# Kernel tuning notes

Hardware: AMD Instinct MI355X
Metric: run time of the kernel (lower is better)

The kernel has to match this reference:

```python
import jax, jax.numpy as jnp
import numpy as np

NUM_HEADS = 16
HEAD_DIM = 64
D_MODEL = NUM_HEADS * HEAD_DIM
EPS = 1e-8
SCALE = 1.0 / np.sqrt(HEAD_DIM)


def setup_inputs() -> dict:
    key = jax.random.key(0)
    ks = jax.random.split(key, 5)
    B, S = 2, 2048
    w_std = 1.0 / np.sqrt(D_MODEL)
    return {
        "x": jax.random.normal(ks[0], (B, S, D_MODEL), dtype=jnp.float32),
        "Wq": jax.random.normal(ks[1], (D_MODEL, D_MODEL), dtype=jnp.float32) * w_std,
        "Wk": jax.random.normal(ks[2], (D_MODEL, D_MODEL), dtype=jnp.float32) * w_std,
        "Wv": jax.random.normal(ks[3], (D_MODEL, D_MODEL), dtype=jnp.float32) * w_std,
        "Wo": jax.random.normal(ks[4], (D_MODEL, D_MODEL), dtype=jnp.float32) * w_std,
        "xsa_scale": jnp.ones((1,), dtype=jnp.float32),
    }


def reference(x, Wq, Wk, Wv, Wo, xsa_scale):
    B, S, _ = x.shape
    # torch nn.Linear(no bias): y = x @ W.T
    def proj(W):
        y = jnp.einsum("bsd,ed->bse", x, W)
        # (B, S, D) -> (B, H, S, Dh)
        return y.reshape(B, S, NUM_HEADS, HEAD_DIM).transpose(0, 2, 1, 3)

    q, k, v = proj(Wq), proj(Wk), proj(Wv)
    scores = jnp.einsum("bhqd,bhkd->bhqk", q, k) * SCALE
    attn = jax.nn.softmax(scores, axis=-1)
    out = jnp.einsum("bhqk,bhkd->bhqd", attn, v)
    # subtract_projection: remove component of out along each token's own v
    dot = jnp.sum(out * v, axis=-1, keepdims=True)
    v_norm_sq = jnp.sum(v * v, axis=-1, keepdims=True) + EPS
    out = out - xsa_scale * (dot / v_norm_sq) * v
    out = out.transpose(0, 2, 1, 3).reshape(B, S, D_MODEL)
    return jnp.einsum("bsd,ed->bse", out, Wo)


if __name__ == "__main__":
    print(reference(**setup_inputs()).shape)
```

## Files before the change

### kernel.cpp

```cpp
#include <hip/hip_runtime.h>
#include <math.h>

#define BATCH 2
#define SEQ   2048
#define NH    16
#define HD    64
#define DM    1024
#define MROWS (BATCH * SEQ)
#define NEL   ((size_t)MROWS * DM)
#define WEL   ((size_t)DM * DM)
#define SM_SCALE_LOG2E 0.18033688011112042f

typedef __bf16 bf16x8 __attribute__((ext_vector_type(8)));
typedef float  f32x4  __attribute__((ext_vector_type(4)));

#define MFMA16(a, b, c) __builtin_amdgcn_mfma_f32_16x16x32_bf16((a), (b), (c), 0, 0, 0)
#define EXP2(x) __builtin_amdgcn_exp2f(x)

#define GLDS16(g, s) __builtin_amdgcn_global_load_lds( \
    (const __attribute__((address_space(1))) void*)(g), \
    (__attribute__((address_space(3))) void*)(s), 16, 0, 0)


__global__ __launch_bounds__(256) void cvt_x(const float* __restrict__ src,
                                             __bf16* __restrict__ dst) {
    const size_t i = ((size_t)blockIdx.x * 256 + threadIdx.x) * 4;
    const float4 f = *(const float4*)&src[i];
    __bf16 b[4] = {(__bf16)f.x, (__bf16)f.y, (__bf16)f.z, (__bf16)f.w};
    *(ushort4*)&dst[i] = *(ushort4*)b;
}

__global__ __launch_bounds__(256) void cvt_w(const float* __restrict__ w0,
                                             const float* __restrict__ w1,
                                             const float* __restrict__ w2,
                                             const float* __restrict__ w3,
                                             __bf16* __restrict__ dst) {
    const int z = blockIdx.z;
    const float* src = (z == 0) ? w0 : (z == 1) ? w1 : (z == 2) ? w2 : w3;
    __bf16* d = dst + (size_t)z * WEL;
    const size_t i = ((size_t)blockIdx.x * 256 + threadIdx.x) * 4;
    const float4 f = *(const float4*)&src[i];
    __bf16 b[4] = {(__bf16)f.x, (__bf16)f.y, (__bf16)f.z, (__bf16)f.w};
    *(ushort4*)&d[i] = *(ushort4*)b;
}

template<int BN>
__global__ __launch_bounds__(256) void gemm_nt_mfma(
    const __bf16* __restrict__ A, const __bf16* __restrict__ W0,
    void* __restrict__ C0, __bf16* __restrict__ Vt, int mode)
{
    constexpr int NI  = BN / 32;
    constexpr int NIT = DM / 32;
    __shared__ __bf16 Ast[2][128 * 32];
    __shared__ __bf16 Bst[2][BN * 32];

    const int t = threadIdx.x;
    const int w = t >> 6, l = t & 63;
    const int quad = l >> 4, l15 = l & 15;
    const int z = blockIdx.z;
    const int m0 = blockIdx.y * 128, n0 = blockIdx.x * BN;
    const int wm = (w >> 1) * 64, wn = (w & 1) * (BN / 2);

    const __bf16* Wp = W0 + (size_t)z * WEL;

    const int lrow = l >> 2;
    const int lkof = ((l & 3) ^ ((lrow >> 1) & 3)) * 8;
    const int qsw = (quad ^ ((l15 >> 1) & 3)) * 8;

    const __bf16* Ag = A + (size_t)(m0 + w * 32 + lrow) * DM + lkof;
    const int aoff = (w * 32) * 32;
    const int brow = (BN == 128) ? (w * 32) : (w * 16);
    const __bf16* Bg = Wp + (size_t)(n0 + brow + lrow) * DM + lkof;
    const int boff = brow * 32;

    f32x4 acc[4][NI];
    #pragma unroll
    for (int i = 0; i < 4; i++)
        #pragma unroll
        for (int j = 0; j < NI; j++) acc[i][j] = (f32x4)0.0f;

    GLDS16(Ag,           &Ast[0][aoff]);
    GLDS16(Ag + 16 * DM, &Ast[0][aoff + 512]);
    GLDS16(Bg,           &Bst[0][boff]);
    if (BN == 128) GLDS16(Bg + 16 * DM, &Bst[0][boff + 512]);
    __syncthreads();

    for (int i = 0; i < NIT; i++) {
        const int cur = i & 1, nxt = cur ^ 1;
        if (i + 1 < NIT) {
            const int k0 = (i + 1) * 32;
            GLDS16(Ag + k0,           &Ast[nxt][aoff]);
            GLDS16(Ag + k0 + 16 * DM, &Ast[nxt][aoff + 512]);
            GLDS16(Bg + k0,           &Bst[nxt][boff]);
            if (BN == 128) GLDS16(Bg + k0 + 16 * DM, &Bst[nxt][boff + 512]);
        }

        bf16x8 af[4], bfr[NI];
        #pragma unroll
        for (int mi = 0; mi < 4; mi++)
            af[mi] = *(const bf16x8*)&Ast[cur][(wm + mi * 16 + l15) * 32 + qsw];
        #pragma unroll
        for (int ni = 0; ni < NI; ni++)
            bfr[ni] = *(const bf16x8*)&Bst[cur][(wn + ni * 16 + l15) * 32 + qsw];
        #pragma unroll
        for (int mi = 0; mi < 4; mi++)
            #pragma unroll
            for (int ni = 0; ni < NI; ni++)
                acc[mi][ni] = MFMA16(af[mi], bfr[ni], acc[mi][ni]);

        __syncthreads();
    }

    if (mode) {
        const float sc = (z == 0) ? SM_SCALE_LOG2E : 1.0f;
        __bf16* C = (__bf16*)C0 + (size_t)z * NEL;
        #pragma unroll
        for (int mi = 0; mi < 4; mi++)
            #pragma unroll
            for (int ni = 0; ni < NI; ni++)
                #pragma unroll
                for (int r = 0; r < 4; r++) {
                    const int row = m0 + wm + mi * 16 + quad * 4 + r;
                    const int col = n0 + wn + ni * 16 + l15;
                    const int b = row >> 11, s = row & (SEQ - 1);
                    const int h = col >> 6,  d = col & (HD - 1);
                    const __bf16 val = (__bf16)(acc[mi][ni][r] * sc);
                    C[((size_t)(b * NH + h) * SEQ + s) * HD + d] = val;
                    if (z == 2)
                        Vt[((size_t)(b * NH + h) * HD + d) * SEQ + s] = val;
                }
    } else {
        float* C = (float*)C0;
        #pragma unroll
        for (int mi = 0; mi < 4; mi++)
            #pragma unroll
            for (int ni = 0; ni < NI; ni++)
                #pragma unroll
                for (int r = 0; r < 4; r++) {
                    const int row = m0 + wm + mi * 16 + quad * 4 + r;
                    const int col = n0 + wn + ni * 16 + l15;
                    C[(size_t)row * DM + col] = acc[mi][ni][r];
                }
    }
}

__global__ __launch_bounds__(256, 3) void attn_mfma(
    const __bf16* __restrict__ Q, const __bf16* __restrict__ K,
    const __bf16* __restrict__ Vt, const __bf16* __restrict__ V,
    const float* __restrict__ xsa, __bf16* __restrict__ X2)
{
    __shared__ __bf16 KV[2][2][2 * 64 * 32];
    __shared__ __bf16 Pt[4][32][64];

    const int t = threadIdx.x;
    const int w = t >> 6, l = t & 63;
    const int quad = l >> 4, l15 = l & 15;
    const int bh = blockIdx.x & 31;
    const int q0 = (blockIdx.x >> 5) * 128;

    const __bf16* Qb  = Q  + (size_t)bh * SEQ * HD;
    const __bf16* Kb  = K  + (size_t)bh * SEQ * HD;
    const __bf16* Vtb = Vt + (size_t)bh * HD * SEQ;

    const int lrow = l >> 2;
    const int lkof = ((l & 3) ^ ((lrow >> 1) & 3)) * 8;
    const int qsw = (quad ^ ((l15 >> 1) & 3)) * 8;
    const int pkey = l15 & 7;

    __bf16* Qst = &KV[1][0][0];
    #pragma unroll
    for (int h = 0; h < 2; h++)
        #pragma unroll
        for (int qq = 0; qq < 2; qq++)
            GLDS16(Qb + (size_t)(q0 + w * 32 + qq * 16 + lrow) * HD + h * 32 + lkof,
                   Qst + h * 4096 + (w * 32 + qq * 16) * 32);
    #pragma unroll
    for (int h = 0; h < 2; h++)
        GLDS16(Kb + (size_t)(w * 16 + lrow) * HD + h * 32 + lkof,
               &KV[0][0][h * 2048 + (w * 16) * 32]);
    #pragma unroll
    for (int kh = 0; kh < 2; kh++)
        GLDS16(Vtb + (size_t)(w * 16 + lrow) * SEQ + kh * 32 + lkof,
               &KV[0][1][kh * 2048 + (w * 16) * 32]);
    __syncthreads();

    bf16x8 qf[2][2];
    #pragma unroll
    for (int h = 0; h < 2; h++)
        #pragma unroll
        for (int mi = 0; mi < 2; mi++)
            qf[h][mi] = *(const bf16x8*)&Qst[h * 4096 +
                          (w * 32 + mi * 16 + l15) * 32 + qsw];
    __syncthreads();

    float l_i[2] = {0.0f, 0.0f};
    f32x4 o[2][4];
    #pragma unroll
    for (int mi = 0; mi < 2; mi++)
        #pragma unroll
        for (int db = 0; db < 4; db++) o[mi][db] = (f32x4)0.0f;

    constexpr int NT = SEQ / 64;
    for (int kt = 0; kt < NT; kt++) {
        const int cur = kt & 1, nxt = cur ^ 1;
        if (kt + 1 < NT) {
            const int k0n = (kt + 1) * 64;
            #pragma unroll
            for (int h = 0; h < 2; h++)
                GLDS16(Kb + (size_t)(k0n + w * 16 + lrow) * HD + h * 32 + lkof,
                       &KV[nxt][0][h * 2048 + (w * 16) * 32]);
            #pragma unroll
            for (int kh = 0; kh < 2; kh++)
                GLDS16(Vtb + (size_t)(w * 16 + lrow) * SEQ + k0n + kh * 32 + lkof,
                       &KV[nxt][1][kh * 2048 + (w * 16) * 32]);
        }
        const __bf16* Ks = &KV[cur][0][0];
        const __bf16* Vs = &KV[cur][1][0];

        f32x4 st[2][4];
        #pragma unroll
        for (int mi = 0; mi < 2; mi++)
            #pragma unroll
            for (int kb = 0; kb < 4; kb++) st[mi][kb] = (f32x4)0.0f;
        #pragma unroll
        for (int h = 0; h < 2; h++)
            #pragma unroll
            for (int kb = 0; kb < 4; kb++) {
                const bf16x8 kf = *(const bf16x8*)&Ks[h * 2048 +
                                      (kb * 16 + l15) * 32 + qsw];
                #pragma unroll
                for (int mi = 0; mi < 2; mi++)
                    st[mi][kb] = MFMA16(kf, qf[h][mi], st[mi][kb]);
            }

        #pragma unroll
        for (int mi = 0; mi < 2; mi++) {
            float rs = 0.0f;
            #pragma unroll
            for (int kb = 0; kb < 4; kb++)
                #pragma unroll
                for (int r = 0; r < 4; r++) {
                    const float p = EXP2(st[mi][kb][r]);
                    st[mi][kb][r] = p;
                    rs += p;
                }
            rs += __shfl_xor(rs, 16);
            rs += __shfl_xor(rs, 32);
            l_i[mi] += rs;
            #pragma unroll
            for (int kb = 0; kb < 4; kb++) {
                __bf16 pb[4] = {(__bf16)st[mi][kb][0], (__bf16)st[mi][kb][1],
                                (__bf16)st[mi][kb][2], (__bf16)st[mi][kb][3]};
                const int pc = ((kb * 2 + (quad >> 1)) ^ pkey) * 8 + (quad & 1) * 4;
                *(uint2*)&Pt[w][mi * 16 + l15][pc] = *(uint2*)pb;
            }
        }

        #pragma unroll
        for (int kh = 0; kh < 2; kh++) {
            bf16x8 pf[2];
            #pragma unroll
            for (int mi = 0; mi < 2; mi++) {
                const int pc = ((kh * 4 + quad) ^ pkey) * 8;
                pf[mi] = *(const bf16x8*)&Pt[w][mi * 16 + l15][pc];
            }
            #pragma unroll
            for (int db = 0; db < 4; db++) {
                const bf16x8 vf = *(const bf16x8*)&Vs[kh * 2048 +
                                      (db * 16 + l15) * 32 + qsw];
                #pragma unroll
                for (int mi = 0; mi < 2; mi++)
                    o[mi][db] = MFMA16(vf, pf[mi], o[mi][db]);
            }
        }

        __syncthreads();
    }

    const float xs = xsa[0];
    const int b = bh >> 4, h = bh & (NH - 1);
    const __bf16* Vb = V + (size_t)bh * SEQ * HD;
    #pragma unroll
    for (int mi = 0; mi < 2; mi++) {
        const int q = q0 + w * 32 + mi * 16 + l15;
        const float inv = 1.0f / l_i[mi];
        float vv[4][4], on[4][4];
        float dp = 0.0f, nn = 0.0f;
        #pragma unroll
        for (int db = 0; db < 4; db++) {
            __bf16 vb4[4];
            *(uint2*)vb4 = *(const uint2*)&Vb[(size_t)q * HD + db * 16 + quad * 4];
            #pragma unroll
            for (int r = 0; r < 4; r++) {
                const float vf = (float)vb4[r];
                const float of = o[mi][db][r] * inv;
                vv[db][r] = vf;
                on[db][r] = of;
                dp += of * vf;
                nn += vf * vf;
            }
        }
        dp += __shfl_xor(dp, 16); dp += __shfl_xor(dp, 32);
        nn += __shfl_xor(nn, 16); nn += __shfl_xor(nn, 32);
        const float coef = xs * dp / (nn + 1e-8f);
        #pragma unroll
        for (int db = 0; db < 4; db++) {
            __bf16 ob[4];
            #pragma unroll
            for (int r = 0; r < 4; r++)
                ob[r] = (__bf16)(on[db][r] - coef * vv[db][r]);
            *(uint2*)&X2[((size_t)b * SEQ + q) * DM + h * HD + db * 16 + quad * 4] =
                *(uint2*)ob;
        }
    }
}

extern "C" void kernel_launch(void* const* d_in, const int* in_sizes, int n_in,
                              void* d_out, int out_size, void* d_ws, size_t ws_size,
                              hipStream_t stream)
{
    (void)in_sizes; (void)n_in; (void)out_size; (void)ws_size;
    const float* x   = (const float*)d_in[0];
    const float* Wq  = (const float*)d_in[1];
    const float* Wk  = (const float*)d_in[2];
    const float* Wv  = (const float*)d_in[3];
    const float* Wo  = (const float*)d_in[4];
    const float* xsa = (const float*)d_in[5];
    float* out = (float*)d_out;

    __bf16* xb  = (__bf16*)d_ws;
    __bf16* Wb  = xb  + NEL;
    __bf16* Qb  = Wb  + 4 * WEL;
    __bf16* Kb  = Qb  + NEL;
    __bf16* Vb  = Kb  + NEL;
    __bf16* Vtb = Vb  + NEL;
    __bf16* X2  = Vtb + NEL;

    cvt_x<<<dim3(NEL / 1024), 256, 0, stream>>>(x, xb);
    cvt_w<<<dim3(WEL / 1024, 1, 4), 256, 0, stream>>>(Wq, Wk, Wv, Wo, Wb);

    gemm_nt_mfma<128><<<dim3(DM / 128, MROWS / 128, 3), 256, 0, stream>>>(
        xb, Wb, Qb, Vtb, 1);

    attn_mfma<<<dim3((SEQ / 128) * BATCH * NH), 256, 0, stream>>>(
        Qb, Kb, Vtb, Vb, xsa, X2);

    gemm_nt_mfma<64><<<dim3(DM / 64, MROWS / 128, 1), 256, 0, stream>>>(
        X2, Wb + 3 * WEL, out, nullptr, 0);
}
```

Measured before the change: 198.7 us.

## Fuse conversion kernels, add MFMA priority hints, halve attention block size

Merges the x and weight bf16 conversion kernels into a single launch to remove one kernel launch. Wraps the MFMA loops in the GEMM and attention kernels with s_setprio so matrix work gets issue priority over other waves. Shrinks attention blocks from 4 to 2 waves (64 queries per block), doubling the grid and having each wave load twice as many K/V rows per tile. The smaller blocks give more blocks for scheduling, but each K/V tile is reused by fewer queries, which raises global load traffic per query.

```diff
diff --git a/kernel.cpp b/kernel.cpp
--- a/kernel.cpp
+++ b/kernel.cpp
@@ -22,26 +22,29 @@
     (__attribute__((address_space(3))) void*)(s), 16, 0, 0)
 
 
-__global__ __launch_bounds__(256) void cvt_x(const float* __restrict__ src,
-                                             __bf16* __restrict__ dst) {
-    const size_t i = ((size_t)blockIdx.x * 256 + threadIdx.x) * 4;
+__global__ __launch_bounds__(256) void cvt_all(
+    const float* __restrict__ x,
+    const float* __restrict__ w0, const float* __restrict__ w1,
+    const float* __restrict__ w2, const float* __restrict__ w3,
+    __bf16* __restrict__ xb, __bf16* __restrict__ wb)
+{
+    const int bid = blockIdx.x;
+    const float* src;
+    __bf16* dst;
+    size_t base;
+    if (bid < 4096) {
+        src = x; dst = xb; base = (size_t)bid * 1024;
+    } else {
+        const int r = bid - 4096;
+        const int z = r >> 10;
+        src = (z == 0) ? w0 : (z == 1) ? w1 : (z == 2) ? w2 : w3;
+        dst = wb + (size_t)z * WEL;
+        base = (size_t)(r & 1023) * 1024;
+    }
+    const size_t i = base + (size_t)threadIdx.x * 4;
     const float4 f = *(const float4*)&src[i];
     __bf16 b[4] = {(__bf16)f.x, (__bf16)f.y, (__bf16)f.z, (__bf16)f.w};
     *(ushort4*)&dst[i] = *(ushort4*)b;
-}
-
-__global__ __launch_bounds__(256) void cvt_w(const float* __restrict__ w0,
-                                             const float* __restrict__ w1,
-                                             const float* __restrict__ w2,
-                                             const float* __restrict__ w3,
-                                             __bf16* __restrict__ dst) {
-    const int z = blockIdx.z;
-    const float* src = (z == 0) ? w0 : (z == 1) ? w1 : (z == 2) ? w2 : w3;
-    __bf16* d = dst + (size_t)z * WEL;
-    const size_t i = ((size_t)blockIdx.x * 256 + threadIdx.x) * 4;
-    const float4 f = *(const float4*)&src[i];
-    __bf16 b[4] = {(__bf16)f.x, (__bf16)f.y, (__bf16)f.z, (__bf16)f.w};
-    *(ushort4*)&d[i] = *(ushort4*)b;
 }
 
 template<int BN>
@@ -102,11 +105,13 @@
         #pragma unroll
         for (int ni = 0; ni < NI; ni++)
             bfr[ni] = *(const bf16x8*)&Bst[cur][(wn + ni * 16 + l15) * 32 + qsw];
+        __builtin_amdgcn_s_setprio(1);
         #pragma unroll
         for (int mi = 0; mi < 4; mi++)
             #pragma unroll
             for (int ni = 0; ni < NI; ni++)
                 acc[mi][ni] = MFMA16(af[mi], bfr[ni], acc[mi][ni]);
+        __builtin_amdgcn_s_setprio(0);
 
         __syncthreads();
     }
@@ -144,19 +149,19 @@
     }
 }
 
-__global__ __launch_bounds__(256, 3) void attn_mfma(
+__global__ __launch_bounds__(128, 2) void attn_mfma(
     const __bf16* __restrict__ Q, const __bf16* __restrict__ K,
     const __bf16* __restrict__ Vt, const __bf16* __restrict__ V,
     const float* __restrict__ xsa, __bf16* __restrict__ X2)
 {
     __shared__ __bf16 KV[2][2][2 * 64 * 32];
-    __shared__ __bf16 Pt[4][32][64];
+    __shared__ __bf16 Pt[2][32][64];
 
     const int t = threadIdx.x;
     const int w = t >> 6, l = t & 63;
     const int quad = l >> 4, l15 = l & 15;
     const int bh = blockIdx.x & 31;
-    const int q0 = (blockIdx.x >> 5) * 128;
+    const int q0 = (blockIdx.x >> 5) * 64;
 
     const __bf16* Qb  = Q  + (size_t)bh * SEQ * HD;
     const __bf16* Kb  = K  + (size_t)bh * SEQ * HD;
@@ -173,15 +178,19 @@
         #pragma unroll
         for (int qq = 0; qq < 2; qq++)
             GLDS16(Qb + (size_t)(q0 + w * 32 + qq * 16 + lrow) * HD + h * 32 + lkof,
-                   Qst + h * 4096 + (w * 32 + qq * 16) * 32);
+                   Qst + h * 2048 + (w * 32 + qq * 16) * 32);
     #pragma unroll
     for (int h = 0; h < 2; h++)
-        GLDS16(Kb + (size_t)(w * 16 + lrow) * HD + h * 32 + lkof,
-               &KV[0][0][h * 2048 + (w * 16) * 32]);
+        #pragma unroll
+        for (int qq = 0; qq < 2; qq++)
+            GLDS16(Kb + (size_t)(w * 32 + qq * 16 + lrow) * HD + h * 32 + lkof,
+                   &KV[0][0][h * 2048 + (w * 32 + qq * 16) * 32]);
     #pragma unroll
     for (int kh = 0; kh < 2; kh++)
-        GLDS16(Vtb + (size_t)(w * 16 + lrow) * SEQ + kh * 32 + lkof,
-               &KV[0][1][kh * 2048 + (w * 16) * 32]);
+        #pragma unroll
+        for (int qq = 0; qq < 2; qq++)
+            GLDS16(Vtb + (size_t)(w * 32 + qq * 16 + lrow) * SEQ + kh * 32 + lkof,
+                   &KV[0][1][kh * 2048 + (w * 32 + qq * 16) * 32]);
     __syncthreads();
 
     bf16x8 qf[2][2];
@@ -189,7 +198,7 @@
     for (int h = 0; h < 2; h++)
         #pragma unroll
         for (int mi = 0; mi < 2; mi++)
-            qf[h][mi] = *(const bf16x8*)&Qst[h * 4096 +
+            qf[h][mi] = *(const bf16x8*)&Qst[h * 2048 +
                           (w * 32 + mi * 16 + l15) * 32 + qsw];
     __syncthreads();
 
@@ -207,12 +216,16 @@
             const int k0n = (kt + 1) * 64;
             #pragma unroll
             for (int h = 0; h < 2; h++)
-                GLDS16(Kb + (size_t)(k0n + w * 16 + lrow) * HD + h * 32 + lkof,
-                       &KV[nxt][0][h * 2048 + (w * 16) * 32]);
+                #pragma unroll
+                for (int qq = 0; qq < 2; qq++)
+                    GLDS16(Kb + (size_t)(k0n + w * 32 + qq * 16 + lrow) * HD + h * 32 + lkof,
+                           &KV[nxt][0][h * 2048 + (w * 32 + qq * 16) * 32]);
             #pragma unroll
             for (int kh = 0; kh < 2; kh++)
-                GLDS16(Vtb + (size_t)(w * 16 + lrow) * SEQ + k0n + kh * 32 + lkof,
-                       &KV[nxt][1][kh * 2048 + (w * 16) * 32]);
+                #pragma unroll
+                for (int qq = 0; qq < 2; qq++)
+                    GLDS16(Vtb + (size_t)(w * 32 + qq * 16 + lrow) * SEQ + k0n + kh * 32 + lkof,
+                           &KV[nxt][1][kh * 2048 + (w * 32 + qq * 16) * 32]);
         }
         const __bf16* Ks = &KV[cur][0][0];
         const __bf16* Vs = &KV[cur][1][0];
@@ -222,6 +235,7 @@
         for (int mi = 0; mi < 2; mi++)
             #pragma unroll
             for (int kb = 0; kb < 4; kb++) st[mi][kb] = (f32x4)0.0f;
+        __builtin_amdgcn_s_setprio(1);
         #pragma unroll
         for (int h = 0; h < 2; h++)
             #pragma unroll
@@ -232,6 +246,7 @@
                 for (int mi = 0; mi < 2; mi++)
                     st[mi][kb] = MFMA16(kf, qf[h][mi], st[mi][kb]);
             }
+        __builtin_amdgcn_s_setprio(0);
 
         #pragma unroll
         for (int mi = 0; mi < 2; mi++) {
@@ -264,6 +279,7 @@
                 const int pc = ((kh * 4 + quad) ^ pkey) * 8;
                 pf[mi] = *(const bf16x8*)&Pt[w][mi * 16 + l15][pc];
             }
+            __builtin_amdgcn_s_setprio(1);
             #pragma unroll
             for (int db = 0; db < 4; db++) {
                 const bf16x8 vf = *(const bf16x8*)&Vs[kh * 2048 +
@@ -272,6 +288,7 @@
                 for (int mi = 0; mi < 2; mi++)
                     o[mi][db] = MFMA16(vf, pf[mi], o[mi][db]);
             }
+            __builtin_amdgcn_s_setprio(0);
         }
 
         __syncthreads();
@@ -336,13 +353,12 @@
     __bf16* Vtb = Vb  + NEL;
     __bf16* X2  = Vtb + NEL;
 
-    cvt_x<<<dim3(NEL / 1024), 256, 0, stream>>>(x, xb);
-    cvt_w<<<dim3(WEL / 1024, 1, 4), 256, 0, stream>>>(Wq, Wk, Wv, Wo, Wb);
+    cvt_all<<<dim3(8192), 256, 0, stream>>>(x, Wq, Wk, Wv, Wo, xb, Wb);
 
     gemm_nt_mfma<128><<<dim3(DM / 128, MROWS / 128, 3), 256, 0, stream>>>(
         xb, Wb, Qb, Vtb, 1);
 
-    attn_mfma<<<dim3((SEQ / 128) * BATCH * NH), 256, 0, stream>>>(
+    attn_mfma<<<dim3((SEQ / 64) * BATCH * NH), 128, 0, stream>>>(
         Qb, Kb, Vtb, Vb, xsa, X2);
 
     gemm_nt_mfma<64><<<dim3(DM / 64, MROWS / 128, 1), 256, 0, stream>>>(
```

After: 197.4 us. No clear change (-0.7%).
